# Kernel tuning notes

Hardware: AMD Instinct MI355X
Metric: run time of the kernel (lower is better)

The kernel has to match this reference:

```python
import jax, jax.numpy as jnp
import numpy as np

NA, NP_, E = 40000, 60000, 80000
D, H = 512, 8
DK = D // H
SQRT_DK = float(DK) ** 0.5


def setup_inputs() -> dict:
    key = jax.random.key(0)
    ks = list(jax.random.split(key, 20))
    it = iter(ks)

    def nrm(shape, scale=1.0):
        return jax.random.normal(next(it), shape, dtype=jnp.float32) * scale

    xav = (6.0 / (DK + DK)) ** 0.5  # xavier_uniform bound for (dk, dk)
    w_scale = D ** -0.5
    inp = {
        "h_author": nrm((NA, D)),
        "h_paper": nrm((NP_, D)),
        "writes_src": jax.random.randint(next(it), (E,), 0, NA, dtype=jnp.int32),
        "writes_dst": jax.random.randint(next(it), (E,), 0, NP_, dtype=jnp.int32),
        "cites_src": jax.random.randint(next(it), (E,), 0, NP_, dtype=jnp.int32),
        "cites_dst": jax.random.randint(next(it), (E,), 0, NP_, dtype=jnp.int32),
        "wb_src": jax.random.randint(next(it), (E,), 0, NP_, dtype=jnp.int32),
        "wb_dst": jax.random.randint(next(it), (E,), 0, NA, dtype=jnp.int32),
        # per-node-type linear weights (2 types: 0=author, 1=paper)
        "Wk": nrm((2, D, D), w_scale), "bk": jnp.zeros((2, D), jnp.float32),
        "Wq": nrm((2, D, D), w_scale), "bq": jnp.zeros((2, D), jnp.float32),
        "Wv": nrm((2, D, D), w_scale), "bv": jnp.zeros((2, D), jnp.float32),
        "Wa": nrm((2, D, D), w_scale), "ba": jnp.zeros((2, D), jnp.float32),
        # per-relation params (3 relations: 0=writes, 1=cites, 2=written_by)
        "rel_att": jax.random.uniform(next(it), (3, H, DK, DK), jnp.float32, -xav, xav),
        "rel_msg": jax.random.uniform(next(it), (3, H, DK, DK), jnp.float32, -xav, xav),
        "rel_pri": jnp.ones((3, H), jnp.float32),
        "skip": jnp.ones((2,), jnp.float32),
    }
    return inp


def _edge_attn_agg(k, q, v, src, dst, pri, n_dst):
    # k, v: (N_src, H, DK) relation-transformed; q: (N_dst, H, DK)
    s = jnp.einsum('ehd,ehd->eh', q[dst], k[src]) * pri / SQRT_DK  # (E, H)
    m = jax.ops.segment_max(s, dst, num_segments=n_dst)            # edge softmax by dst
    ex = jnp.exp(s - m[dst])
    den = jax.ops.segment_sum(ex, dst, num_segments=n_dst)
    a = ex / den[dst]
    return jax.ops.segment_sum(v[src] * a[:, :, None], dst, num_segments=n_dst)


def reference(h_author, h_paper, writes_src, writes_dst, cites_src, cites_dst,
              wb_src, wb_dst, Wk, bk, Wq, bq, Wv, bv, Wa, ba,
              rel_att, rel_msg, rel_pri, skip):
    def proj(h, W, b, t):
        return (h @ W[t] + b[t]).reshape(-1, H, DK)

    k_a, v_a, q_a = proj(h_author, Wk, bk, 0), proj(h_author, Wv, bv, 0), proj(h_author, Wq, bq, 0)
    k_p, v_p, q_p = proj(h_paper, Wk, bk, 1), proj(h_paper, Wv, bv, 1), proj(h_paper, Wq, bq, 1)

    def rel(k, v, r):
        return (jnp.einsum('nhd,hde->nhe', k, rel_att[r]),
                jnp.einsum('nhd,hde->nhe', v, rel_msg[r]))

    k0, v0 = rel(k_a, v_a, 0)  # writes: author -> paper
    agg_w = _edge_attn_agg(k0, q_p, v0, writes_src, writes_dst, rel_pri[0], NP_)
    k1, v1 = rel(k_p, v_p, 1)  # cites: paper -> paper
    agg_c = _edge_attn_agg(k1, q_p, v1, cites_src, cites_dst, rel_pri[1], NP_)
    k2, v2 = rel(k_p, v_p, 2)  # written_by: paper -> author
    agg_b = _edge_attn_agg(k2, q_a, v2, wb_src, wb_dst, rel_pri[2], NA)

    t_paper = ((agg_w + agg_c) * 0.5).reshape(NP_, D)  # cross_reducer='mean'
    t_author = agg_b.reshape(NA, D)

    alpha = jax.nn.sigmoid(skip)
    out_a = (t_author @ Wa[0] + ba[0]) * alpha[0] + h_author * (1.0 - alpha[0])
    out_p = (t_paper @ Wa[1] + ba[1]) * alpha[1] + h_paper * (1.0 - alpha[1])
    return out_a, out_p
```

## Files before the change

### kernel.cpp

```cpp
#include <hip/hip_runtime.h>
#include <math.h>

#define D_ 512
#define H_ 8

typedef short bf16x8 __attribute__((ext_vector_type(8)));
typedef float f32x4 __attribute__((ext_vector_type(4)));

__device__ __forceinline__ unsigned short f2bf(float x) {
  unsigned int u = __float_as_uint(x);
  unsigned int r = (u + 0x7fff + ((u >> 16) & 1)) >> 16;
  return (unsigned short)r;
}
__device__ __forceinline__ float bf2f(unsigned short b) {
  return __uint_as_float(((unsigned int)b) << 16);
}

struct PrepArgs {
  const float *hA, *hP;
  unsigned short *hA16, *hP16;
  const float *fWin[6], *fbin[6], *frel[6];
  unsigned short *fWf[6];
  float *fbf[6];
  const float *tW[4];
  unsigned short *tWt[4];
  const float *cin[2];
  float *cout[2];
  int *degree;
  int NT;
  int b1, b2, b3, b4, b5;
};

__global__ __launch_bounds__(512) void prep_kernel(PrepArgs p) {
  const int b = blockIdx.x, t = threadIdx.x;
  if (b < p.b2) {
    const float* in; unsigned short* out; long i;
    if (b < p.b1) { in = p.hA; out = p.hA16; i = (long)b * 512 + t; }
    else          { in = p.hP; out = p.hP16; i = (long)(b - p.b1) * 512 + t; }
    float4 a = ((const float4*)in)[i * 2];
    float4 c = ((const float4*)in)[i * 2 + 1];
    bf16x8 o;
    o[0] = (short)f2bf(a.x); o[1] = (short)f2bf(a.y);
    o[2] = (short)f2bf(a.z); o[3] = (short)f2bf(a.w);
    o[4] = (short)f2bf(c.x); o[5] = (short)f2bf(c.y);
    o[6] = (short)f2bf(c.z); o[7] = (short)f2bf(c.w);
    ((bf16x8*)out)[i] = o;
  } else if (b < p.b3) {
    int idx = b - p.b2;
    int job = idx / 513, row = idx - job * 513;
    int h = t >> 6, e = t & 63;
    const float* src = (row < D_) ? (p.fWin[job] + (long)row * D_) : p.fbin[job];
    const float* rl = p.frel[job] + h * 64 * 64;
    float acc = 0.f;
#pragma unroll 16
    for (int d = 0; d < 64; ++d)
      acc = fmaf(src[h * 64 + d], rl[d * 64 + e], acc);
    if (row < D_) p.fWf[job][(long)t * D_ + row] = f2bf(acc);
    else p.fbf[job][t] = acc;
  } else if (b < p.b4) {
    int idx = b - p.b3;
    int job = idx >> 9, n = idx & 511;
    p.tWt[job][(long)n * D_ + t] = f2bf(p.tW[job][(long)t * D_ + n]);
  } else if (b < p.b5) {
    int job = b - p.b4;
    p.cout[job][t] = p.cin[job][t];
  } else {
    int i = (b - p.b5) * 512 + t;
    if (i < p.NT) p.degree[i] = 0;
  }
}

__global__ void hist_kernel(const int* __restrict__ w_dst,
                            const int* __restrict__ c_dst,
                            const int* __restrict__ b_dst,
                            int* __restrict__ degree, int E, int NP) {
  int i = blockIdx.x * blockDim.x + threadIdx.x;
  if (i >= 3 * E) return;
  int r = i / E, e = i - r * E;
  int d, base;
  if (r == 0)      { d = w_dst[e]; base = 0; }
  else if (r == 1) { d = c_dst[e]; base = NP; }
  else             { d = b_dst[e]; base = 2 * NP; }
  atomicAdd(degree + base + d, 1);
}

__global__ void scan1_kernel(const int* __restrict__ in, int* __restrict__ out,
                             int* __restrict__ aux, int n) {
  __shared__ int tmp[256];
  int t = threadIdx.x;
  int i = blockIdx.x * 256 + t;
  int v = (i < n) ? in[i] : 0;
  tmp[t] = v;
  __syncthreads();
#pragma unroll
  for (int d = 1; d < 256; d <<= 1) {
    int add = (t >= d) ? tmp[t - d] : 0;
    __syncthreads();
    tmp[t] += add;
    __syncthreads();
  }
  if (i < n) out[i] = tmp[t] - v;
  if (t == 255) aux[blockIdx.x] = tmp[255];
}

__global__ void scan2_kernel(int* __restrict__ aux, int nb) {
  __shared__ int tmp[1024];
  int t = threadIdx.x;
  int v = (t < nb) ? aux[t] : 0;
  tmp[t] = v;
  __syncthreads();
#pragma unroll
  for (int d = 1; d < 1024; d <<= 1) {
    int add = (t >= d) ? tmp[t - d] : 0;
    __syncthreads();
    tmp[t] += add;
    __syncthreads();
  }
  if (t < nb) aux[t] = tmp[t] - v;
}

__global__ void scan3_kernel(int* __restrict__ starts, int* __restrict__ cursor,
                             const int* __restrict__ aux, int n) {
  int i = blockIdx.x * 256 + threadIdx.x;
  if (i >= n) return;
  int s = starts[i] + aux[blockIdx.x];
  starts[i] = s;
  cursor[i] = s;
}

__global__ void scatter_kernel(const int* __restrict__ w_src, const int* __restrict__ w_dst,
                               const int* __restrict__ c_src, const int* __restrict__ c_dst,
                               const int* __restrict__ b_src, const int* __restrict__ b_dst,
                               int* __restrict__ cursor, int* __restrict__ csr,
                               int E, int NP) {
  int i = blockIdx.x * blockDim.x + threadIdx.x;
  if (i >= 3 * E) return;
  int r = i / E, e = i - r * E;
  int s, d, base;
  if (r == 0)      { s = w_src[e]; d = w_dst[e]; base = 0; }
  else if (r == 1) { s = c_src[e]; d = c_dst[e]; base = NP; }
  else             { s = b_src[e]; d = b_dst[e]; base = 2 * NP; }
  int pos = atomicAdd(cursor + base + d, 1);
  csr[pos] = s;
}

__global__ __launch_bounds__(256) void attn_all(
    const unsigned short* __restrict__ Pq,
    const unsigned short* __restrict__ Akw, const unsigned short* __restrict__ Avw,
    const unsigned short* __restrict__ Pkc, const unsigned short* __restrict__ Pvc,
    const unsigned short* __restrict__ Aq,
    const unsigned short* __restrict__ Pkb, const unsigned short* __restrict__ Pvb,
    const int* __restrict__ csr, const int* __restrict__ starts,
    const int* __restrict__ degree, const float* __restrict__ pri,
    unsigned short* __restrict__ t16, int NP, int NA, int NAp) {
  long gid = (long)blockIdx.x * blockDim.x + threadIdx.x;
  int gw = (int)(gid >> 6);
  if (gw >= NP + NAp) return;
  int lane = threadIdx.x & 63;
  int h = lane >> 3, off = (lane & 7) << 3;

  const unsigned short* q;
  long orow;
  int node;
  const int paper = gw < NP;
  if (paper) {
    node = gw; q = Pq;
    orow = (long)(NAp + node) * D_ + h * 64 + off;
  } else {
    int aw = gw - NP;
    orow = (long)aw * D_ + h * 64 + off;
    if (aw >= NA) {
      bf16x8 z;
#pragma unroll
      for (int r = 0; r < 8; ++r) z[r] = 0;
      *(bf16x8*)(t16 + orow) = z;
      return;
    }
    node = aw; q = Aq;
  }

  bf16x8 qv = *(const bf16x8*)(q + (long)node * D_ + h * 64 + off);
  float qf[8];
#pragma unroll
  for (int r = 0; r < 8; ++r) qf[r] = bf2f((unsigned short)qv[r]);

  float res[8] = {};

  auto process = [&](const unsigned short* K, const unsigned short* V,
                     int nodeabs, float ps) {
    int st = starts[nodeabs], dg = degree[nodeabs];
    float m = -INFINITY, l = 0.f;
    float acc[8] = {};
    for (int i = 0; i < dg; ++i) {
      int s = csr[st + i];
      const long ro = (long)s * D_ + h * 64 + off;
      bf16x8 kv = *(const bf16x8*)(K + ro);
      bf16x8 vv = *(const bf16x8*)(V + ro);
      float dot = 0.f;
#pragma unroll
      for (int r = 0; r < 8; ++r)
        dot = fmaf(qf[r], bf2f((unsigned short)kv[r]), dot);
      dot += __shfl_xor(dot, 1);
      dot += __shfl_xor(dot, 2);
      dot += __shfl_xor(dot, 4);
      float sc = dot * ps;
      float mn = fmaxf(m, sc);
      float scale = __expf(m - mn);
      float pv = __expf(sc - mn);
      l = l * scale + pv;
#pragma unroll
      for (int r = 0; r < 8; ++r)
        acc[r] = acc[r] * scale + pv * bf2f((unsigned short)vv[r]);
      m = mn;
    }
    if (l > 0.f) {
      float inv = 1.f / l;
#pragma unroll
      for (int r = 0; r < 8; ++r) res[r] += acc[r] * inv;
    }
  };

  float outscale;
  if (paper) {
    process(Akw, Avw, node, pri[h] * 0.125f);
    process(Pkc, Pvc, NP + node, pri[8 + h] * 0.125f);
    outscale = 0.5f;
  } else {
    process(Pkb, Pvb, 2 * NP + node, pri[16 + h] * 0.125f);
    outscale = 1.0f;
  }

  bf16x8 o;
#pragma unroll
  for (int r = 0; r < 8; ++r) o[r] = (short)f2bf(res[r] * outscale);
  *(bf16x8*)(t16 + orow) = o;
}

__device__ __forceinline__ void gload_lds16(const void* g, void* l) {
  __builtin_amdgcn_global_load_lds(
      (const __attribute__((address_space(1))) void*)g,
      (__attribute__((address_space(3))) void*)l, 16, 0, 0);
}

struct ProjArgs {
  const unsigned short *A0, *A1;
  const unsigned short *B0, *B1;
  const float *bias0, *bias1;
  void* outs[8];
  int M0, M1, split;
};

struct OutArgs {
  const unsigned short* A;
  const unsigned short *B0, *B1;
  const float *bias0, *bias1;
  const float *H0, *H1;
  const float* skip;
  float *o0, *o1;
  int mtsplit, NAp, M0, M1;
};

#define GEMM_CORE(A_PTR, B_PTR)                                               \
  f32x4 acc[4][4] = {};                                                       \
  const int rr = lane & 15;                                                   \
  const int rx = (rr & 7) << 4;                                               \
  auto STAGE_PART = [&](int u, int part) {                                    \
    const int sl = u % 3;                                                     \
    const int k0 = u * 64 + swz;                                              \
    if (part == 0) {                                                          \
      _Pragma("unroll")                                                       \
      for (int i = 0; i < 2; ++i) {                                           \
        int gr = bm + srow + i * 64;                                          \
        if (gr >= M) gr = M - 1;                                              \
        gload_lds16((A_PTR) + (long)gr * D_ + k0,                             \
                    &As[sl][i * 4096 + wave * 512]);                          \
      }                                                                       \
      int gb = bn + srow;                                                     \
      gload_lds16((B_PTR) + (long)gb * D_ + k0, &Bs[sl][wave * 512]);         \
    } else {                                                                  \
      _Pragma("unroll")                                                       \
      for (int i = 2; i < 4; ++i) {                                           \
        int gr = bm + srow + i * 64;                                          \
        if (gr >= M) gr = M - 1;                                              \
        gload_lds16((A_PTR) + (long)gr * D_ + k0,                             \
                    &As[sl][i * 4096 + wave * 512]);                          \
      }                                                                       \
      int gb = bn + 64 + srow;                                                \
      gload_lds16((B_PTR) + (long)gb * D_ + k0, &Bs[sl][4096 + wave * 512]);  \
    }                                                                         \
  };                                                                          \
  STAGE_PART(0, 0); STAGE_PART(0, 1);                                         \
  STAGE_PART(1, 0); STAGE_PART(1, 1);                                         \
  _Pragma("unroll")                                                           \
  for (int t = 0; t < 8; ++t) {                                               \
    if (t < 7) asm volatile("s_waitcnt vmcnt(6)" ::: "memory");               \
    else       asm volatile("s_waitcnt vmcnt(0)" ::: "memory");               \
    __builtin_amdgcn_s_barrier();                                             \
    asm volatile("" ::: "memory");                                            \
    const int sslot = t % 3;                                                  \
    const char* ab = (const char*)&As[sslot][0];                              \
    const char* bb = (const char*)&Bs[sslot][0];                              \
    _Pragma("unroll")                                                         \
    for (int kk = 0; kk < 2; ++kk) {                                          \
      const int cs = (kk * 64 + (lane >> 4) * 16) ^ rx;                       \
      bf16x8 af[4], bfr[4];                                                   \
      _Pragma("unroll")                                                       \
      for (int mi = 0; mi < 4; ++mi)                                          \
        af[mi] = *(const bf16x8*)(ab + (wm + mi * 16 + rr) * 128 + cs);       \
      _Pragma("unroll")                                                       \
      for (int nj = 0; nj < 4; ++nj)                                          \
        bfr[nj] = *(const bf16x8*)(bb + (wn + nj * 16 + rr) * 128 + cs);      \
      if (t < 6) STAGE_PART(t + 2, kk);                                       \
      __builtin_amdgcn_s_setprio(1);                                          \
      _Pragma("unroll")                                                       \
      for (int mi = 0; mi < 4; ++mi)                                          \
        _Pragma("unroll")                                                     \
        for (int nj = 0; nj < 4; ++nj)                                        \
          acc[mi][nj] = __builtin_amdgcn_mfma_f32_16x16x32_bf16(              \
              af[mi], bfr[nj], acc[mi][nj], 0, 0, 0);                         \
      __builtin_amdgcn_s_setprio(0);                                          \
      asm volatile("" ::: "memory");                                          \
      if (kk == 0) {                                                          \
        __builtin_amdgcn_s_barrier();                                         \
        asm volatile("" ::: "memory");                                        \
      }                                                                       \
    }                                                                         \
  }

__global__ __launch_bounds__(512, 2) void gemm_proj(ProjArgs pa) {
  __shared__ unsigned short As[3][256 * 64];
  __shared__ unsigned short Bs[3][128 * 64];

  const int nwg = gridDim.x, orig = blockIdx.x;
  const int q8 = nwg >> 3, r8 = nwg & 7;
  const int xcd = orig & 7, pos = orig >> 3;
  const int wgid =
      (xcd < r8 ? xcd * (q8 + 1) : r8 * (q8 + 1) + (xcd - r8) * q8) + pos;

  int reg, mt, nt;
  if (wgid < pa.split) { reg = 0; mt = wgid / 12; nt = wgid - mt * 12; }
  else { int r = wgid - pa.split; reg = 1; mt = r / 20; nt = r - mt * 20; }
  const unsigned short* A  = reg ? pa.A1 : pa.A0;
  const unsigned short* Bt = reg ? pa.B1 : pa.B0;
  const float* bias = reg ? pa.bias1 : pa.bias0;
  const int M = reg ? pa.M1 : pa.M0;
  const int bm = mt * 256, bn = nt * 128;

  const int tid = threadIdx.x;
  const int wave = tid >> 6, lane = tid & 63;
  const int wm = (wave >> 1) * 64;
  const int wn = (wave & 1) * 64;
  const int srow = tid >> 3;
  const int swz = ((tid & 7) ^ (srow & 7)) * 8;

  GEMM_CORE(A, Bt)

  const int cr = (lane >> 4) * 4;
  const int cc = lane & 15;
  const int matu = (bn + wn) >> 9;
  const int wcb = (bn + wn) & 511;
  unsigned short* ob16 = (unsigned short*)pa.outs[(reg ? 3 : 0) + matu];
#pragma unroll
  for (int mi = 0; mi < 4; ++mi) {
    int rowb = bm + wm + mi * 16 + cr;
#pragma unroll
    for (int nj = 0; nj < 4; ++nj) {
      float bb = bias[bn + wn + nj * 16 + cc];
#pragma unroll
      for (int r = 0; r < 4; ++r) {
        int row = rowb + r;
        if (row >= M) continue;
        ob16[(long)row * D_ + wcb + nj * 16 + cc] = f2bf(acc[mi][nj][r] + bb);
      }
    }
  }
}

__global__ __launch_bounds__(512, 2) void gemm_out(OutArgs oa) {
  __shared__ unsigned short As[3][256 * 64];
  __shared__ unsigned short Bs[3][128 * 64];

  const int nwg = gridDim.x, orig = blockIdx.x;
  const int q8 = nwg >> 3, r8 = nwg & 7;
  const int xcd = orig & 7, pos = orig >> 3;
  const int wgid =
      (xcd < r8 ? xcd * (q8 + 1) : r8 * (q8 + 1) + (xcd - r8) * q8) + pos;

  const int bmt = wgid >> 2;
  const int bn = (wgid & 3) * 128;
  const int reg = bmt >= oa.mtsplit;
  const int bm = (reg ? bmt - oa.mtsplit : bmt) * 256;
  const int abase = reg ? oa.NAp : 0;
  const int M = reg ? oa.M1 : oa.M0;
  const unsigned short* Aeff = oa.A + (long)abase * D_;
  const unsigned short* Bt = reg ? oa.B1 : oa.B0;
  const float* bias = reg ? oa.bias1 : oa.bias0;
  const float* Hres = reg ? oa.H1 : oa.H0;
  float* outp = reg ? oa.o1 : oa.o0;

  const int tid = threadIdx.x;
  const int wave = tid >> 6, lane = tid & 63;
  const int wm = (wave >> 1) * 64;
  const int wn = (wave & 1) * 64;
  const int srow = tid >> 3;
  const int swz = ((tid & 7) ^ (srow & 7)) * 8;

  GEMM_CORE(Aeff, Bt)

  float sv = oa.skip[reg];
  float alpha = 1.f / (1.f + expf(-sv));
  float beta = 1.f - alpha;
  const int cr = (lane >> 4) * 4;
  const int cc = lane & 15;
#pragma unroll
  for (int mi = 0; mi < 4; ++mi) {
    int rowb = bm + wm + mi * 16 + cr;
#pragma unroll
    for (int nj = 0; nj < 4; ++nj) {
      int col = bn + wn + nj * 16 + cc;
      float bb = bias[col];
#pragma unroll
      for (int r = 0; r < 4; ++r) {
        int row = rowb + r;
        if (row >= M) continue;
        float val = acc[mi][nj][r] + bb;
        val = val * alpha + Hres[(long)row * D_ + col] * beta;
        outp[(long)row * D_ + col] = val;
      }
    }
  }
}

extern "C" void kernel_launch(void* const* d_in, const int* in_sizes, int n_in,
                              void* d_out, int out_size, void* d_ws, size_t ws_size,
                              hipStream_t stream) {
  const float* h_author = (const float*)d_in[0];
  const float* h_paper  = (const float*)d_in[1];
  const int* w_src = (const int*)d_in[2];
  const int* w_dst = (const int*)d_in[3];
  const int* c_src = (const int*)d_in[4];
  const int* c_dst = (const int*)d_in[5];
  const int* b_src = (const int*)d_in[6];
  const int* b_dst = (const int*)d_in[7];
  const float* Wk = (const float*)d_in[8];
  const float* bk = (const float*)d_in[9];
  const float* Wq = (const float*)d_in[10];
  const float* bq = (const float*)d_in[11];
  const float* Wv = (const float*)d_in[12];
  const float* bv = (const float*)d_in[13];
  const float* Wa = (const float*)d_in[14];
  const float* ba = (const float*)d_in[15];
  const float* rel_att = (const float*)d_in[16];
  const float* rel_msg = (const float*)d_in[17];
  const float* rel_pri = (const float*)d_in[18];
  const float* skip = (const float*)d_in[19];

  const int NA = in_sizes[0] / D_;
  const int NP = in_sizes[1] / D_;
  const int E  = in_sizes[2];
  const int NT = 2 * NP + NA;
  const int tA = (NA + 255) / 256;
  const int tP = (NP + 255) / 256;
  const int NAp = tA * 256;

  char* w = (char*)d_ws;
  auto alloc = [&](long bytes) {
    char* p = w;
    w += (bytes + 255) & ~255L;
    return p;
  };
  unsigned short* hA16 = (unsigned short*)alloc((long)NA * D_ * 2);
  unsigned short* hP16 = (unsigned short*)alloc((long)NP * D_ * 2);
  unsigned short* Pq   = (unsigned short*)alloc((long)NP * D_ * 2);
  unsigned short* Pkc  = (unsigned short*)alloc((long)NP * D_ * 2);
  unsigned short* Pvc  = (unsigned short*)alloc((long)NP * D_ * 2);
  unsigned short* Pkb  = (unsigned short*)alloc((long)NP * D_ * 2);
  unsigned short* Pvb  = (unsigned short*)alloc((long)NP * D_ * 2);
  unsigned short* Aq   = (unsigned short*)alloc((long)NA * D_ * 2);
  unsigned short* Akw  = (unsigned short*)alloc((long)NA * D_ * 2);
  unsigned short* Avw  = (unsigned short*)alloc((long)NA * D_ * 2);
  unsigned short* t16  = (unsigned short*)alloc((long)(NAp + NP) * D_ * 2);
  unsigned short* BtP  = (unsigned short*)alloc((long)2560 * D_ * 2);
  unsigned short* BtA  = (unsigned short*)alloc((long)1536 * D_ * 2);
  float* bfP           = (float*)alloc(2560 * 4);
  float* bfA           = (float*)alloc(1536 * 4);
  unsigned short* Wa0t = (unsigned short*)alloc((long)D_ * D_ * 2);
  unsigned short* Wa1t = (unsigned short*)alloc((long)D_ * D_ * 2);
  int* degree          = (int*)alloc((long)NT * 4);
  int* starts          = (int*)alloc((long)NT * 4);
  int* cursor          = (int*)alloc((long)NT * 4);
  int* csr             = (int*)alloc((long)3 * E * 4);
  int* aux             = (int*)alloc(((long)NT / 256 + 2) * 4);

  const long WD = (long)D_ * D_;
  const long RS = (long)H_ * 64 * 64;
  const long SEG = (long)D_ * D_;

  float* out_a = (float*)d_out;
  float* out_p = out_a + (long)NA * D_;

  {
    PrepArgs p;
    p.hA = h_author; p.hP = h_paper; p.hA16 = hA16; p.hP16 = hP16;
    p.fWin[0] = Wk + WD; p.fbin[0] = bk + D_; p.frel[0] = rel_att + RS;
    p.fWf[0] = BtP + SEG;     p.fbf[0] = bfP + 512;
    p.fWin[1] = Wv + WD; p.fbin[1] = bv + D_; p.frel[1] = rel_msg + RS;
    p.fWf[1] = BtP + 2 * SEG; p.fbf[1] = bfP + 1024;
    p.fWin[2] = Wk + WD; p.fbin[2] = bk + D_; p.frel[2] = rel_att + 2 * RS;
    p.fWf[2] = BtP + 3 * SEG; p.fbf[2] = bfP + 1536;
    p.fWin[3] = Wv + WD; p.fbin[3] = bv + D_; p.frel[3] = rel_msg + 2 * RS;
    p.fWf[3] = BtP + 4 * SEG; p.fbf[3] = bfP + 2048;
    p.fWin[4] = Wk;      p.fbin[4] = bk;      p.frel[4] = rel_att;
    p.fWf[4] = BtA + SEG;     p.fbf[4] = bfA + 512;
    p.fWin[5] = Wv;      p.fbin[5] = bv;      p.frel[5] = rel_msg;
    p.fWf[5] = BtA + 2 * SEG; p.fbf[5] = bfA + 1024;
    p.tW[0] = Wq + WD; p.tWt[0] = BtP;
    p.tW[1] = Wq;      p.tWt[1] = BtA;
    p.tW[2] = Wa;      p.tWt[2] = Wa0t;
    p.tW[3] = Wa + WD; p.tWt[3] = Wa1t;
    p.cin[0] = bq + D_; p.cout[0] = bfP;
    p.cin[1] = bq;      p.cout[1] = bfA;
    p.degree = degree; p.NT = NT;
    p.b1 = NA / 8;
    p.b2 = p.b1 + NP / 8;
    p.b3 = p.b2 + 6 * 513;
    p.b4 = p.b3 + 4 * 512;
    p.b5 = p.b4 + 2;
    int total = p.b5 + (NT + 511) / 512;
    prep_kernel<<<total, 512, 0, stream>>>(p);
  }

  {
    int th = 3 * E;
    hist_kernel<<<(th + 255) / 256, 256, 0, stream>>>(w_dst, c_dst, b_dst,
                                                      degree, E, NP);
    int nb = (NT + 255) / 256;
    scan1_kernel<<<nb, 256, 0, stream>>>(degree, starts, aux, NT);
    scan2_kernel<<<1, 1024, 0, stream>>>(aux, nb);
    scan3_kernel<<<nb, 256, 0, stream>>>(starts, cursor, aux, NT);
    scatter_kernel<<<(th + 255) / 256, 256, 0, stream>>>(
        w_src, w_dst, c_src, c_dst, b_src, b_dst, cursor, csr, E, NP);
  }

  {
    ProjArgs pa;
    pa.A0 = hA16; pa.A1 = hP16;
    pa.B0 = BtA;  pa.B1 = BtP;
    pa.bias0 = bfA; pa.bias1 = bfP;
    pa.outs[0] = Aq;  pa.outs[1] = Akw; pa.outs[2] = Avw;
    pa.outs[3] = Pq;  pa.outs[4] = Pkc; pa.outs[5] = Pvc;
    pa.outs[6] = Pkb; pa.outs[7] = Pvb;
    pa.M0 = NA; pa.M1 = NP;
    pa.split = tA * 12;
    int nwg = pa.split + tP * 20;
    gemm_proj<<<nwg, 512, 0, stream>>>(pa);
  }

  {
    long th = (long)(NP + NAp) * 64;
    attn_all<<<(int)((th + 255) / 256), 256, 0, stream>>>(
        Pq, Akw, Avw, Pkc, Pvc, Aq, Pkb, Pvb,
        csr, starts, degree, rel_pri, t16, NP, NA, NAp);
  }

  {
    OutArgs oa;
    oa.A = t16;
    oa.B0 = Wa0t; oa.B1 = Wa1t;
    oa.bias0 = ba; oa.bias1 = ba + D_;
    oa.H0 = h_author; oa.H1 = h_paper;
    oa.skip = skip;
    oa.o0 = out_a; oa.o1 = out_p;
    oa.mtsplit = tA; oa.NAp = NAp; oa.M0 = NA; oa.M1 = NP;
    int nwg = (tA + tP) * 4;
    gemm_out<<<nwg, 512, 0, stream>>>(oa);
  }
}
```

Baseline: 954.3 us.

## Enlarge GEMM tiles to 256x256 with ping-pong double-buffered quadrant schedule

Both GEMM kernels now use 256x256 output tiles instead of 256x128, so each wave computes a 128x64 sub-tile (8x4 accumulators). The three-stage LDS pipeline becomes a two-slot double buffer in which loads of the next K tile are interleaved between four barrier-separated MFMA quadrants. The goal is higher arithmetic intensity and fewer global/LDS loads per FLOP. In exchange it doubles accumulator registers (which may hurt occupancy under launch bounds of 2) and halves the number of workgroups, which can leave CUs idle.

```diff
diff --git a/kernel.cpp b/kernel.cpp
--- a/kernel.cpp
+++ b/kernel.cpp
@@ -242,6 +242,115 @@
       (__attribute__((address_space(3))) void*)l, 16, 0, 0);
 }
 
+#define BARRIER_ do { __builtin_amdgcn_s_barrier(); asm volatile("" ::: "memory"); } while (0)
+
+#define RD_A(dst, base, mio)                                                  \
+  _Pragma("unroll")                                                           \
+  for (int kk = 0; kk < 2; ++kk) {                                            \
+    const int cs = (kk * 64 + qkb) ^ rx;                                      \
+    _Pragma("unroll")                                                         \
+    for (int mi = 0; mi < 4; ++mi)                                            \
+      dst[kk * 4 + mi] = *(const bf16x8*)((base) +                            \
+          (wm + (mi + (mio)) * 16 + rr) * 128 + cs);                          \
+  }
+
+#define RD_B(dst, base, njo)                                                  \
+  _Pragma("unroll")                                                           \
+  for (int kk = 0; kk < 2; ++kk) {                                            \
+    const int cs = (kk * 64 + qkb) ^ rx;                                      \
+    _Pragma("unroll")                                                         \
+    for (int nj = 0; nj < 2; ++nj)                                            \
+      dst[kk * 2 + nj] = *(const bf16x8*)((base) +                            \
+          (wn + (nj + (njo)) * 16 + rr) * 128 + cs);                          \
+  }
+
+#define MFMA_Q(af, bf_, mio, njo)                                             \
+  __builtin_amdgcn_s_setprio(1);                                              \
+  _Pragma("unroll")                                                           \
+  for (int kk = 0; kk < 2; ++kk)                                              \
+    _Pragma("unroll")                                                         \
+    for (int mi = 0; mi < 4; ++mi)                                            \
+      _Pragma("unroll")                                                       \
+      for (int nj = 0; nj < 2; ++nj)                                          \
+        acc[mi + (mio)][nj + (njo)] =                                         \
+            __builtin_amdgcn_mfma_f32_16x16x32_bf16(                          \
+                af[kk * 4 + mi], bf_[kk * 2 + nj],                            \
+                acc[mi + (mio)][nj + (njo)], 0, 0, 0);                        \
+  __builtin_amdgcn_s_setprio(0);
+
+#define GEMM_CORE(A_PTR, B_PTR)                                               \
+  f32x4 acc[8][4] = {};                                                       \
+  const int rr = lane & 15;                                                   \
+  const int rx = (rr & 7) << 4;                                               \
+  const int qkb = (lane >> 4) * 16;                                           \
+  bf16x8 aLo[8], aHi[8], bLo[4], bHi[4];                                      \
+  auto STAGE_A = [&](int slot, int tile, int half) {                          \
+    const int k0 = tile * 64 + swz;                                           \
+    _Pragma("unroll")                                                         \
+    for (int j = 0; j < 2; ++j) {                                             \
+      int gr = bm + half * 128 + srow + j * 64;                               \
+      if (gr >= M) gr = M - 1;                                                \
+      gload_lds16((A_PTR) + (long)gr * D_ + k0,                               \
+                  &As[slot][half * 8192 + j * 4096 + wave * 512]);            \
+    }                                                                         \
+  };                                                                          \
+  auto STAGE_B = [&](int slot, int tile, int half) {                          \
+    const int k0 = tile * 64 + swz;                                           \
+    _Pragma("unroll")                                                         \
+    for (int j = 0; j < 2; ++j) {                                             \
+      int gr = bn + half * 128 + srow + j * 64;                               \
+      gload_lds16((B_PTR) + (long)gr * D_ + k0,                               \
+                  &Bs[slot][half * 8192 + j * 4096 + wave * 512]);            \
+    }                                                                         \
+  };                                                                          \
+                \
+  STAGE_B(0, 0, 0); STAGE_B(0, 0, 1); STAGE_A(0, 0, 0); STAGE_A(0, 0, 1);     \
+  STAGE_B(1, 1, 0); STAGE_B(1, 1, 1);                                         \
+  asm volatile("s_waitcnt vmcnt(4)" ::: "memory");                            \
+  BARRIER_;                                                                   \
+  {                                                                           \
+    const char* a0_ = (const char*)&As[0][0];                                 \
+    const char* b0_ = (const char*)&Bs[0][0];                                 \
+    const char* a1_ = (const char*)&As[1][0];                                 \
+    const char* b1_ = (const char*)&Bs[1][0];                                 \
+    _Pragma("unroll")                                                         \
+    for (int it = 0; it < 4; ++it) {                                          \
+      const int ta = 2 * it, tb = ta + 1;                                     \
+                                   \
+      RD_A(aLo, a0_, 0) RD_B(bLo, b0_, 0)                                     \
+      STAGE_A(1, tb, 0);                                                      \
+      BARRIER_; MFMA_Q(aLo, bLo, 0, 0) BARRIER_;                              \
+      RD_B(bHi, b0_, 2)                                                       \
+      STAGE_A(1, tb, 1);                                                      \
+      BARRIER_; MFMA_Q(aLo, bHi, 0, 2) BARRIER_;                              \
+      RD_A(aHi, a0_, 4)                                                       \
+      if (ta + 2 < 8) STAGE_B(0, ta + 2, 0);                                  \
+      BARRIER_; MFMA_Q(aHi, bLo, 4, 0) BARRIER_;                              \
+      if (ta + 2 < 8) {                                                       \
+        STAGE_B(0, ta + 2, 1);                                                \
+        asm volatile("s_waitcnt vmcnt(4)" ::: "memory");                      \
+      } else {                                                                \
+        asm volatile("s_waitcnt vmcnt(0)" ::: "memory");                      \
+      }                                                                       \
+      BARRIER_; MFMA_Q(aHi, bHi, 4, 2) BARRIER_;                              \
+                                   \
+      RD_A(aLo, a1_, 0) RD_B(bLo, b1_, 0)                                     \
+      if (ta + 2 < 8) STAGE_A(0, ta + 2, 0);                                  \
+      BARRIER_; MFMA_Q(aLo, bLo, 0, 0) BARRIER_;                              \
+      RD_B(bHi, b1_, 2)                                                       \
+      if (ta + 2 < 8) STAGE_A(0, ta + 2, 1);                                  \
+      BARRIER_; MFMA_Q(aLo, bHi, 0, 2) BARRIER_;                              \
+      RD_A(aHi, a1_, 4)                                                       \
+      if (tb + 2 < 8) STAGE_B(1, tb + 2, 0);                                  \
+      BARRIER_; MFMA_Q(aHi, bLo, 4, 0) BARRIER_;                              \
+      if (tb + 2 < 8) {                                                       \
+        STAGE_B(1, tb + 2, 1);                                                \
+        asm volatile("s_waitcnt vmcnt(4)" ::: "memory");                      \
+      }                                                                       \
+      BARRIER_; MFMA_Q(aHi, bHi, 4, 2) BARRIER_;                              \
+    }                                                                         \
+  }
+
 struct ProjArgs {
   const unsigned short *A0, *A1;
   const unsigned short *B0, *B1;
@@ -260,76 +369,9 @@
   int mtsplit, NAp, M0, M1;
 };
 
-#define GEMM_CORE(A_PTR, B_PTR)                                               \
-  f32x4 acc[4][4] = {};                                                       \
-  const int rr = lane & 15;                                                   \
-  const int rx = (rr & 7) << 4;                                               \
-  auto STAGE_PART = [&](int u, int part) {                                    \
-    const int sl = u % 3;                                                     \
-    const int k0 = u * 64 + swz;                                              \
-    if (part == 0) {                                                          \
-      _Pragma("unroll")                                                       \
-      for (int i = 0; i < 2; ++i) {                                           \
-        int gr = bm + srow + i * 64;                                          \
-        if (gr >= M) gr = M - 1;                                              \
-        gload_lds16((A_PTR) + (long)gr * D_ + k0,                             \
-                    &As[sl][i * 4096 + wave * 512]);                          \
-      }                                                                       \
-      int gb = bn + srow;                                                     \
-      gload_lds16((B_PTR) + (long)gb * D_ + k0, &Bs[sl][wave * 512]);         \
-    } else {                                                                  \
-      _Pragma("unroll")                                                       \
-      for (int i = 2; i < 4; ++i) {                                           \
-        int gr = bm + srow + i * 64;                                          \
-        if (gr >= M) gr = M - 1;                                              \
-        gload_lds16((A_PTR) + (long)gr * D_ + k0,                             \
-                    &As[sl][i * 4096 + wave * 512]);                          \
-      }                                                                       \
-      int gb = bn + 64 + srow;                                                \
-      gload_lds16((B_PTR) + (long)gb * D_ + k0, &Bs[sl][4096 + wave * 512]);  \
-    }                                                                         \
-  };                                                                          \
-  STAGE_PART(0, 0); STAGE_PART(0, 1);                                         \
-  STAGE_PART(1, 0); STAGE_PART(1, 1);                                         \
-  _Pragma("unroll")                                                           \
-  for (int t = 0; t < 8; ++t) {                                               \
-    if (t < 7) asm volatile("s_waitcnt vmcnt(6)" ::: "memory");               \
-    else       asm volatile("s_waitcnt vmcnt(0)" ::: "memory");               \
-    __builtin_amdgcn_s_barrier();                                             \
-    asm volatile("" ::: "memory");                                            \
-    const int sslot = t % 3;                                                  \
-    const char* ab = (const char*)&As[sslot][0];                              \
-    const char* bb = (const char*)&Bs[sslot][0];                              \
-    _Pragma("unroll")                                                         \
-    for (int kk = 0; kk < 2; ++kk) {                                          \
-      const int cs = (kk * 64 + (lane >> 4) * 16) ^ rx;                       \
-      bf16x8 af[4], bfr[4];                                                   \
-      _Pragma("unroll")                                                       \
-      for (int mi = 0; mi < 4; ++mi)                                          \
-        af[mi] = *(const bf16x8*)(ab + (wm + mi * 16 + rr) * 128 + cs);       \
-      _Pragma("unroll")                                                       \
-      for (int nj = 0; nj < 4; ++nj)                                          \
-        bfr[nj] = *(const bf16x8*)(bb + (wn + nj * 16 + rr) * 128 + cs);      \
-      if (t < 6) STAGE_PART(t + 2, kk);                                       \
-      __builtin_amdgcn_s_setprio(1);                                          \
-      _Pragma("unroll")                                                       \
-      for (int mi = 0; mi < 4; ++mi)                                          \
-        _Pragma("unroll")                                                     \
-        for (int nj = 0; nj < 4; ++nj)                                        \
-          acc[mi][nj] = __builtin_amdgcn_mfma_f32_16x16x32_bf16(              \
-              af[mi], bfr[nj], acc[mi][nj], 0, 0, 0);                         \
-      __builtin_amdgcn_s_setprio(0);                                          \
-      asm volatile("" ::: "memory");                                          \
-      if (kk == 0) {                                                          \
-        __builtin_amdgcn_s_barrier();                                         \
-        asm volatile("" ::: "memory");                                        \
-      }                                                                       \
-    }                                                                         \
-  }
-
 __global__ __launch_bounds__(512, 2) void gemm_proj(ProjArgs pa) {
-  __shared__ unsigned short As[3][256 * 64];
-  __shared__ unsigned short Bs[3][128 * 64];
+  __shared__ unsigned short As[2][256 * 64];
+  __shared__ unsigned short Bs[2][256 * 64];
 
   const int nwg = gridDim.x, orig = blockIdx.x;
   const int q8 = nwg >> 3, r8 = nwg & 7;
@@ -338,18 +380,18 @@
       (xcd < r8 ? xcd * (q8 + 1) : r8 * (q8 + 1) + (xcd - r8) * q8) + pos;
 
   int reg, mt, nt;
-  if (wgid < pa.split) { reg = 0; mt = wgid / 12; nt = wgid - mt * 12; }
-  else { int r = wgid - pa.split; reg = 1; mt = r / 20; nt = r - mt * 20; }
+  if (wgid < pa.split) { reg = 0; mt = wgid / 6; nt = wgid - mt * 6; }
+  else { int r = wgid - pa.split; reg = 1; mt = r / 10; nt = r - mt * 10; }
   const unsigned short* A  = reg ? pa.A1 : pa.A0;
   const unsigned short* Bt = reg ? pa.B1 : pa.B0;
   const float* bias = reg ? pa.bias1 : pa.bias0;
   const int M = reg ? pa.M1 : pa.M0;
-  const int bm = mt * 256, bn = nt * 128;
+  const int bm = mt * 256, bn = nt * 256;
 
   const int tid = threadIdx.x;
   const int wave = tid >> 6, lane = tid & 63;
-  const int wm = (wave >> 1) * 64;
-  const int wn = (wave & 1) * 64;
+  const int wm = (wave >> 2) * 128;
+  const int wn = (wave & 3) * 64;
   const int srow = tid >> 3;
   const int swz = ((tid & 7) ^ (srow & 7)) * 8;
 
@@ -361,7 +403,7 @@
   const int wcb = (bn + wn) & 511;
   unsigned short* ob16 = (unsigned short*)pa.outs[(reg ? 3 : 0) + matu];
 #pragma unroll
-  for (int mi = 0; mi < 4; ++mi) {
+  for (int mi = 0; mi < 8; ++mi) {
     int rowb = bm + wm + mi * 16 + cr;
 #pragma unroll
     for (int nj = 0; nj < 4; ++nj) {
@@ -377,8 +419,8 @@
 }
 
 __global__ __launch_bounds__(512, 2) void gemm_out(OutArgs oa) {
-  __shared__ unsigned short As[3][256 * 64];
-  __shared__ unsigned short Bs[3][128 * 64];
+  __shared__ unsigned short As[2][256 * 64];
+  __shared__ unsigned short Bs[2][256 * 64];
 
   const int nwg = gridDim.x, orig = blockIdx.x;
   const int q8 = nwg >> 3, r8 = nwg & 7;
@@ -386,8 +428,8 @@
   const int wgid =
       (xcd < r8 ? xcd * (q8 + 1) : r8 * (q8 + 1) + (xcd - r8) * q8) + pos;
 
-  const int bmt = wgid >> 2;
-  const int bn = (wgid & 3) * 128;
+  const int bmt = wgid >> 1;
+  const int bn = (wgid & 1) * 256;
   const int reg = bmt >= oa.mtsplit;
   const int bm = (reg ? bmt - oa.mtsplit : bmt) * 256;
   const int abase = reg ? oa.NAp : 0;
@@ -400,8 +442,8 @@
 
   const int tid = threadIdx.x;
   const int wave = tid >> 6, lane = tid & 63;
-  const int wm = (wave >> 1) * 64;
-  const int wn = (wave & 1) * 64;
+  const int wm = (wave >> 2) * 128;
+  const int wn = (wave & 3) * 64;
   const int srow = tid >> 3;
   const int swz = ((tid & 7) ^ (srow & 7)) * 8;
 
@@ -413,7 +455,7 @@
   const int cr = (lane >> 4) * 4;
   const int cc = lane & 15;
 #pragma unroll
-  for (int mi = 0; mi < 4; ++mi) {
+  for (int mi = 0; mi < 8; ++mi) {
     int rowb = bm + wm + mi * 16 + cr;
 #pragma unroll
     for (int nj = 0; nj < 4; ++nj) {
@@ -551,8 +593,8 @@
     pa.outs[3] = Pq;  pa.outs[4] = Pkc; pa.outs[5] = Pvc;
     pa.outs[6] = Pkb; pa.outs[7] = Pvb;
     pa.M0 = NA; pa.M1 = NP;
-    pa.split = tA * 12;
-    int nwg = pa.split + tP * 20;
+    pa.split = tA * 6;
+    int nwg = pa.split + tP * 10;
     gemm_proj<<<nwg, 512, 0, stream>>>(pa);
   }
 
@@ -572,7 +614,7 @@
     oa.skip = skip;
     oa.o0 = out_a; oa.o1 = out_p;
     oa.mtsplit = tA; oa.NAp = NAp; oa.M0 = NA; oa.M1 = NP;
-    int nwg = (tA + tP) * 4;
+    int nwg = (tA + tP) * 2;
     gemm_out<<<nwg, 512, 0, stream>>>(oa);
   }
 }
```

New measurement: 935.3 us. 2.0% less time.

## Prepack GEMM weights into MFMA fragment order and load B directly from global

Applied to the files above, without the earlier changes.

Weights are written during prep in a packed layout matching the MFMA B-fragment lane order, so the GEMM kernels read B fragments straight from global/L2 into registers instead of staging them through LDS. The workgroup tile shrinks from 256x128 with 512 threads to 128x128 with 256 threads, and only A is staged through a three-slot LDS ring, with fewer barriers per k-step. This cuts LDS use and traffic and should allow more workgroups per CU. The cost is per-lane global loads of B on the critical path, relying on cache hits for the small shared weight matrices, and each tile reuses B across fewer rows.

```diff
diff --git a/kernel.cpp b/kernel.cpp
--- a/kernel.cpp
+++ b/kernel.cpp
@@ -16,14 +16,21 @@
   return __uint_as_float(((unsigned int)b) << 16);
 }
 
+__device__ __forceinline__ long pk_idx(int n, int k) {
+  int nt = n >> 7, njj = (n >> 4) & 7, rl = n & 15;
+  int kt = k >> 6, kk = (k >> 5) & 1, q = (k >> 3) & 3, e = k & 7;
+  return ((((long)(nt * 8 + kt) * 2 + kk) * 8 + njj) * 64 + (q * 16 + rl)) * 8 + e;
+}
+
 struct PrepArgs {
   const float *hA, *hP;
   unsigned short *hA16, *hP16;
   const float *fWin[6], *fbin[6], *frel[6];
-  unsigned short *fWf[6];
+  unsigned short *fpk[6];
+  int fnoff[6];
   float *fbf[6];
   const float *tW[4];
-  unsigned short *tWt[4];
+  unsigned short *tpk[4];
   const float *cin[2];
   float *cout[2];
   int *degree;
@@ -55,12 +62,12 @@
 #pragma unroll 16
     for (int d = 0; d < 64; ++d)
       acc = fmaf(src[h * 64 + d], rl[d * 64 + e], acc);
-    if (row < D_) p.fWf[job][(long)t * D_ + row] = f2bf(acc);
+    if (row < D_) p.fpk[job][pk_idx(p.fnoff[job] + t, row)] = f2bf(acc);
     else p.fbf[job][t] = acc;
   } else if (b < p.b4) {
     int idx = b - p.b3;
     int job = idx >> 9, n = idx & 511;
-    p.tWt[job][(long)n * D_ + t] = f2bf(p.tW[job][(long)t * D_ + n]);
+    p.tpk[job][pk_idx(n, t)] = f2bf(p.tW[job][(long)t * D_ + n]);
   } else if (b < p.b5) {
     int job = b - p.b4;
     p.cout[job][t] = p.cin[job][t];
@@ -242,9 +249,62 @@
       (__attribute__((address_space(3))) void*)l, 16, 0, 0);
 }
 
+#define GEMM_CORE(A_PTR, PK_PTR)                                              \
+  f32x4 acc[4][4] = {};                                                       \
+  const int rr = lane & 15;                                                   \
+  const int qk = lane >> 4;                                                   \
+  const int rx = (rr & 7) << 4;                                               \
+  auto STAGE_A = [&](int slot, int tile) {                                    \
+    const int k0 = tile * 64 + swz;                                           \
+    _Pragma("unroll")                                                         \
+    for (int j = 0; j < 4; ++j) {                                             \
+      int gr = bm + srow + j * 32;                                            \
+      if (gr >= M) gr = M - 1;                                                \
+      gload_lds16((A_PTR) + (long)gr * D_ + k0,                               \
+                  &As[slot][j * 2048 + wave * 512]);                          \
+    }                                                                         \
+  };                                                                          \
+  STAGE_A(0, 0); STAGE_A(1, 1);                                               \
+  _Pragma("unroll")                                                           \
+  for (int t = 0; t < 8; ++t) {                                               \
+    asm volatile("s_waitcnt vmcnt(4)" ::: "memory");                          \
+    __builtin_amdgcn_s_barrier();                                             \
+    asm volatile("" ::: "memory");                                            \
+    bf16x8 bfr[8];                                                            \
+    _Pragma("unroll")                                                         \
+    for (int kk = 0; kk < 2; ++kk)                                            \
+      _Pragma("unroll")                                                       \
+      for (int nj = 0; nj < 4; ++nj)                                          \
+        bfr[kk * 4 + nj] = *(const bf16x8*)((PK_PTR) +                        \
+            ((long)((nt * 8 + t) * 16 + kk * 8 + (wn >> 4) + nj) * 64 +       \
+             lane) * 8);                                                      \
+    bf16x8 af[8];                                                             \
+    const char* ab = (const char*)&As[t % 3][0];                              \
+    _Pragma("unroll")                                                         \
+    for (int kk = 0; kk < 2; ++kk) {                                          \
+      const int cs = (kk * 64 + qk * 16) ^ rx;                                \
+      _Pragma("unroll")                                                       \
+      for (int mi = 0; mi < 4; ++mi)                                          \
+        af[kk * 4 + mi] =                                                     \
+            *(const bf16x8*)(ab + (wm + mi * 16 + rr) * 128 + cs);            \
+    }                                                                         \
+    if (t + 2 < 8) STAGE_A((t + 2) % 3, t + 2);                               \
+    __builtin_amdgcn_s_setprio(1);                                            \
+    _Pragma("unroll")                                                         \
+    for (int kk = 0; kk < 2; ++kk)                                            \
+      _Pragma("unroll")                                                       \
+      for (int mi = 0; mi < 4; ++mi)                                          \
+        _Pragma("unroll")                                                     \
+        for (int nj = 0; nj < 4; ++nj)                                        \
+          acc[mi][nj] = __builtin_amdgcn_mfma_f32_16x16x32_bf16(              \
+              af[kk * 4 + mi], bfr[kk * 4 + nj], acc[mi][nj], 0, 0, 0);       \
+    __builtin_amdgcn_s_setprio(0);                                            \
+    asm volatile("" ::: "memory");                                            \
+  }
+
 struct ProjArgs {
   const unsigned short *A0, *A1;
-  const unsigned short *B0, *B1;
+  const unsigned short *PK0, *PK1;
   const float *bias0, *bias1;
   void* outs[8];
   int M0, M1, split;
@@ -252,7 +312,7 @@
 
 struct OutArgs {
   const unsigned short* A;
-  const unsigned short *B0, *B1;
+  const unsigned short *PK0, *PK1;
   const float *bias0, *bias1;
   const float *H0, *H1;
   const float* skip;
@@ -260,76 +320,8 @@
   int mtsplit, NAp, M0, M1;
 };
 
-#define GEMM_CORE(A_PTR, B_PTR)                                               \
-  f32x4 acc[4][4] = {};                                                       \
-  const int rr = lane & 15;                                                   \
-  const int rx = (rr & 7) << 4;                                               \
-  auto STAGE_PART = [&](int u, int part) {                                    \
-    const int sl = u % 3;                                                     \
-    const int k0 = u * 64 + swz;                                              \
-    if (part == 0) {                                                          \
-      _Pragma("unroll")                                                       \
-      for (int i = 0; i < 2; ++i) {                                           \
-        int gr = bm + srow + i * 64;                                          \
-        if (gr >= M) gr = M - 1;                                              \
-        gload_lds16((A_PTR) + (long)gr * D_ + k0,                             \
-                    &As[sl][i * 4096 + wave * 512]);                          \
-      }                                                                       \
-      int gb = bn + srow;                                                     \
-      gload_lds16((B_PTR) + (long)gb * D_ + k0, &Bs[sl][wave * 512]);         \
-    } else {                                                                  \
-      _Pragma("unroll")                                                       \
-      for (int i = 2; i < 4; ++i) {                                           \
-        int gr = bm + srow + i * 64;                                          \
-        if (gr >= M) gr = M - 1;                                              \
-        gload_lds16((A_PTR) + (long)gr * D_ + k0,                             \
-                    &As[sl][i * 4096 + wave * 512]);                          \
-      }                                                                       \
-      int gb = bn + 64 + srow;                                                \
-      gload_lds16((B_PTR) + (long)gb * D_ + k0, &Bs[sl][4096 + wave * 512]);  \
-    }                                                                         \
-  };                                                                          \
-  STAGE_PART(0, 0); STAGE_PART(0, 1);                                         \
-  STAGE_PART(1, 0); STAGE_PART(1, 1);                                         \
-  _Pragma("unroll")                                                           \
-  for (int t = 0; t < 8; ++t) {                                               \
-    if (t < 7) asm volatile("s_waitcnt vmcnt(6)" ::: "memory");               \
-    else       asm volatile("s_waitcnt vmcnt(0)" ::: "memory");               \
-    __builtin_amdgcn_s_barrier();                                             \
-    asm volatile("" ::: "memory");                                            \
-    const int sslot = t % 3;                                                  \
-    const char* ab = (const char*)&As[sslot][0];                              \
-    const char* bb = (const char*)&Bs[sslot][0];                              \
-    _Pragma("unroll")                                                         \
-    for (int kk = 0; kk < 2; ++kk) {                                          \
-      const int cs = (kk * 64 + (lane >> 4) * 16) ^ rx;                       \
-      bf16x8 af[4], bfr[4];                                                   \
-      _Pragma("unroll")                                                       \
-      for (int mi = 0; mi < 4; ++mi)                                          \
-        af[mi] = *(const bf16x8*)(ab + (wm + mi * 16 + rr) * 128 + cs);       \
-      _Pragma("unroll")                                                       \
-      for (int nj = 0; nj < 4; ++nj)                                          \
-        bfr[nj] = *(const bf16x8*)(bb + (wn + nj * 16 + rr) * 128 + cs);      \
-      if (t < 6) STAGE_PART(t + 2, kk);                                       \
-      __builtin_amdgcn_s_setprio(1);                                          \
-      _Pragma("unroll")                                                       \
-      for (int mi = 0; mi < 4; ++mi)                                          \
-        _Pragma("unroll")                                                     \
-        for (int nj = 0; nj < 4; ++nj)                                        \
-          acc[mi][nj] = __builtin_amdgcn_mfma_f32_16x16x32_bf16(              \
-              af[mi], bfr[nj], acc[mi][nj], 0, 0, 0);                         \
-      __builtin_amdgcn_s_setprio(0);                                          \
-      asm volatile("" ::: "memory");                                          \
-      if (kk == 0) {                                                          \
-        __builtin_amdgcn_s_barrier();                                         \
-        asm volatile("" ::: "memory");                                        \
-      }                                                                       \
-    }                                                                         \
-  }
-
-__global__ __launch_bounds__(512, 2) void gemm_proj(ProjArgs pa) {
-  __shared__ unsigned short As[3][256 * 64];
-  __shared__ unsigned short Bs[3][128 * 64];
+__global__ __launch_bounds__(256, 3) void gemm_proj(ProjArgs pa) {
+  __shared__ unsigned short As[3][128 * 64];
 
   const int nwg = gridDim.x, orig = blockIdx.x;
   const int q8 = nwg >> 3, r8 = nwg & 7;
@@ -341,10 +333,10 @@
   if (wgid < pa.split) { reg = 0; mt = wgid / 12; nt = wgid - mt * 12; }
   else { int r = wgid - pa.split; reg = 1; mt = r / 20; nt = r - mt * 20; }
   const unsigned short* A  = reg ? pa.A1 : pa.A0;
-  const unsigned short* Bt = reg ? pa.B1 : pa.B0;
+  const unsigned short* PK = reg ? pa.PK1 : pa.PK0;
   const float* bias = reg ? pa.bias1 : pa.bias0;
   const int M = reg ? pa.M1 : pa.M0;
-  const int bm = mt * 256, bn = nt * 128;
+  const int bm = mt * 128, bn = nt * 128;
 
   const int tid = threadIdx.x;
   const int wave = tid >> 6, lane = tid & 63;
@@ -353,7 +345,7 @@
   const int srow = tid >> 3;
   const int swz = ((tid & 7) ^ (srow & 7)) * 8;
 
-  GEMM_CORE(A, Bt)
+  GEMM_CORE(A, PK)
 
   const int cr = (lane >> 4) * 4;
   const int cc = lane & 15;
@@ -376,9 +368,8 @@
   }
 }
 
-__global__ __launch_bounds__(512, 2) void gemm_out(OutArgs oa) {
-  __shared__ unsigned short As[3][256 * 64];
-  __shared__ unsigned short Bs[3][128 * 64];
+__global__ __launch_bounds__(256, 3) void gemm_out(OutArgs oa) {
+  __shared__ unsigned short As[3][128 * 64];
 
   const int nwg = gridDim.x, orig = blockIdx.x;
   const int q8 = nwg >> 3, r8 = nwg & 7;
@@ -387,13 +378,14 @@
       (xcd < r8 ? xcd * (q8 + 1) : r8 * (q8 + 1) + (xcd - r8) * q8) + pos;
 
   const int bmt = wgid >> 2;
-  const int bn = (wgid & 3) * 128;
+  const int nt = wgid & 3;
+  const int bn = nt * 128;
   const int reg = bmt >= oa.mtsplit;
-  const int bm = (reg ? bmt - oa.mtsplit : bmt) * 256;
+  const int bm = (reg ? bmt - oa.mtsplit : bmt) * 128;
   const int abase = reg ? oa.NAp : 0;
   const int M = reg ? oa.M1 : oa.M0;
-  const unsigned short* Aeff = oa.A + (long)abase * D_;
-  const unsigned short* Bt = reg ? oa.B1 : oa.B0;
+  const unsigned short* A  = oa.A + (long)abase * D_;
+  const unsigned short* PK = reg ? oa.PK1 : oa.PK0;
   const float* bias = reg ? oa.bias1 : oa.bias0;
   const float* Hres = reg ? oa.H1 : oa.H0;
   float* outp = reg ? oa.o1 : oa.o0;
@@ -405,7 +397,7 @@
   const int srow = tid >> 3;
   const int swz = ((tid & 7) ^ (srow & 7)) * 8;
 
-  GEMM_CORE(Aeff, Bt)
+  GEMM_CORE(A, PK)
 
   float sv = oa.skip[reg];
   float alpha = 1.f / (1.f + expf(-sv));
@@ -459,9 +451,9 @@
   const int NP = in_sizes[1] / D_;
   const int E  = in_sizes[2];
   const int NT = 2 * NP + NA;
-  const int tA = (NA + 255) / 256;
-  const int tP = (NP + 255) / 256;
-  const int NAp = tA * 256;
+  const int tA = (NA + 127) / 128;
+  const int tP = (NP + 127) / 128;
+  const int NAp = tA * 128;
 
   char* w = (char*)d_ws;
   auto alloc = [&](long bytes) {
@@ -480,12 +472,12 @@
   unsigned short* Akw  = (unsigned short*)alloc((long)NA * D_ * 2);
   unsigned short* Avw  = (unsigned short*)alloc((long)NA * D_ * 2);
   unsigned short* t16  = (unsigned short*)alloc((long)(NAp + NP) * D_ * 2);
-  unsigned short* BtP  = (unsigned short*)alloc((long)2560 * D_ * 2);
-  unsigned short* BtA  = (unsigned short*)alloc((long)1536 * D_ * 2);
+  unsigned short* PKP  = (unsigned short*)alloc((long)2560 * D_ * 2);
+  unsigned short* PKA  = (unsigned short*)alloc((long)1536 * D_ * 2);
   float* bfP           = (float*)alloc(2560 * 4);
   float* bfA           = (float*)alloc(1536 * 4);
-  unsigned short* Wa0t = (unsigned short*)alloc((long)D_ * D_ * 2);
-  unsigned short* Wa1t = (unsigned short*)alloc((long)D_ * D_ * 2);
+  unsigned short* PK0  = (unsigned short*)alloc((long)D_ * D_ * 2);
+  unsigned short* PK1  = (unsigned short*)alloc((long)D_ * D_ * 2);
   int* degree          = (int*)alloc((long)NT * 4);
   int* starts          = (int*)alloc((long)NT * 4);
   int* cursor          = (int*)alloc((long)NT * 4);
@@ -494,7 +486,6 @@
 
   const long WD = (long)D_ * D_;
   const long RS = (long)H_ * 64 * 64;
-  const long SEG = (long)D_ * D_;
 
   float* out_a = (float*)d_out;
   float* out_p = out_a + (long)NA * D_;
@@ -503,21 +494,21 @@
     PrepArgs p;
     p.hA = h_author; p.hP = h_paper; p.hA16 = hA16; p.hP16 = hP16;
     p.fWin[0] = Wk + WD; p.fbin[0] = bk + D_; p.frel[0] = rel_att + RS;
-    p.fWf[0] = BtP + SEG;     p.fbf[0] = bfP + 512;
+    p.fpk[0] = PKP; p.fnoff[0] = 512;  p.fbf[0] = bfP + 512;
     p.fWin[1] = Wv + WD; p.fbin[1] = bv + D_; p.frel[1] = rel_msg + RS;
-    p.fWf[1] = BtP + 2 * SEG; p.fbf[1] = bfP + 1024;
+    p.fpk[1] = PKP; p.fnoff[1] = 1024; p.fbf[1] = bfP + 1024;
     p.fWin[2] = Wk + WD; p.fbin[2] = bk + D_; p.frel[2] = rel_att + 2 * RS;
-    p.fWf[2] = BtP + 3 * SEG; p.fbf[2] = bfP + 1536;
+    p.fpk[2] = PKP; p.fnoff[2] = 1536; p.fbf[2] = bfP + 1536;
     p.fWin[3] = Wv + WD; p.fbin[3] = bv + D_; p.frel[3] = rel_msg + 2 * RS;
-    p.fWf[3] = BtP + 4 * SEG; p.fbf[3] = bfP + 2048;
+    p.fpk[3] = PKP; p.fnoff[3] = 2048; p.fbf[3] = bfP + 2048;
     p.fWin[4] = Wk;      p.fbin[4] = bk;      p.frel[4] = rel_att;
-    p.fWf[4] = BtA + SEG;     p.fbf[4] = bfA + 512;
+    p.fpk[4] = PKA; p.fnoff[4] = 512;  p.fbf[4] = bfA + 512;
     p.fWin[5] = Wv;      p.fbin[5] = bv;      p.frel[5] = rel_msg;
-    p.fWf[5] = BtA + 2 * SEG; p.fbf[5] = bfA + 1024;
-    p.tW[0] = Wq + WD; p.tWt[0] = BtP;
-    p.tW[1] = Wq;      p.tWt[1] = BtA;
-    p.tW[2] = Wa;      p.tWt[2] = Wa0t;
-    p.tW[3] = Wa + WD; p.tWt[3] = Wa1t;
+    p.fpk[5] = PKA; p.fnoff[5] = 1024; p.fbf[5] = bfA + 1024;
+    p.tW[0] = Wq + WD; p.tpk[0] = PKP;
+    p.tW[1] = Wq;      p.tpk[1] = PKA;
+    p.tW[2] = Wa;      p.tpk[2] = PK0;
+    p.tW[3] = Wa + WD; p.tpk[3] = PK1;
     p.cin[0] = bq + D_; p.cout[0] = bfP;
     p.cin[1] = bq;      p.cout[1] = bfA;
     p.degree = degree; p.NT = NT;
@@ -545,7 +536,7 @@
   {
     ProjArgs pa;
     pa.A0 = hA16; pa.A1 = hP16;
-    pa.B0 = BtA;  pa.B1 = BtP;
+    pa.PK0 = PKA; pa.PK1 = PKP;
     pa.bias0 = bfA; pa.bias1 = bfP;
     pa.outs[0] = Aq;  pa.outs[1] = Akw; pa.outs[2] = Avw;
     pa.outs[3] = Pq;  pa.outs[4] = Pkc; pa.outs[5] = Pvc;
@@ -553,7 +544,7 @@
     pa.M0 = NA; pa.M1 = NP;
     pa.split = tA * 12;
     int nwg = pa.split + tP * 20;
-    gemm_proj<<<nwg, 512, 0, stream>>>(pa);
+    gemm_proj<<<nwg, 256, 0, stream>>>(pa);
   }
 
   {
@@ -566,13 +557,13 @@
   {
     OutArgs oa;
     oa.A = t16;
-    oa.B0 = Wa0t; oa.B1 = Wa1t;
+    oa.PK0 = PK0; oa.PK1 = PK1;
     oa.bias0 = ba; oa.bias1 = ba + D_;
     oa.H0 = h_author; oa.H1 = h_paper;
     oa.skip = skip;
     oa.o0 = out_a; oa.o1 = out_p;
     oa.mtsplit = tA; oa.NAp = NAp; oa.M0 = NA; oa.M1 = NP;
     int nwg = (tA + tP) * 4;
-    gemm_out<<<nwg, 512, 0, stream>>>(oa);
-  }
-}
+    gemm_out<<<nwg, 256, 0, stream>>>(oa);
+  }
+}
```

After: 885.5 us (median of 5 runs). -7.2%, faster.
